# Kernel tuning notes

Measured on AMD Instinct MI355X. Metric: run time of the kernel, lower is better.

## Reference

```python
import jax, jax.numpy as jnp
import numpy as np

B, S, D, K = 16, 4096, 256, 1024


def setup_inputs() -> dict:
    key = jax.random.key(0)
    k1, k2 = jax.random.split(key)
    z_e = jax.random.normal(k1, (B, S, D), dtype=jnp.float32)
    # nn.Embedding weight initialized uniform(-1/K, 1/K)
    codebook = jax.random.uniform(k2, (K, D), dtype=jnp.float32,
                                  minval=-1.0 / K, maxval=1.0 / K)
    return {"z_e": z_e, "codebook": codebook}


def reference(z_e, codebook):
    # straight_through path of VQEmbedding
    d = codebook.shape[1]
    x = z_e.reshape(-1, d)                                   # [N, D]
    dist = (jnp.sum(x * x, axis=1, keepdims=True)
            + jnp.sum(codebook * codebook, axis=1)
            - 2.0 * (x @ codebook.T))                        # [N, K]
    idx = jnp.argmin(dist, axis=1)                           # [N]
    codes = jnp.take(codebook, idx, axis=0).reshape(z_e.shape)  # gather
    z_q = z_e + jax.lax.stop_gradient(codes - z_e)           # straight-through codes (detached codebook)
    z_q_bar = codes                                          # codes with grad to codebook
    return (z_q, z_q_bar)
```

## Files before the change

kernel.cpp:

```cpp
#include <hip/hip_runtime.h>
#include <stdint.h>

#define D 256
#define KCODES 1024
#define NROWS 65536

using int4v  = __attribute__((ext_vector_type(4))) int;
using int16v = __attribute__((ext_vector_type(16))) int;

__device__ __forceinline__ float rne_f(float x) { return __builtin_rintf(x); }

__device__ __forceinline__ void gl_lds16(const void* g, void* l) {
  __builtin_amdgcn_global_load_lds(
      (const __attribute__((address_space(1))) void*)g,
      (__attribute__((address_space(3))) void*)l, 16, 0, 0);
}

__device__ __forceinline__ void dig4(float t, int* d) {
  float f0 = rne_f(t);  float t1 = __fmul_rn(__fsub_rn(t, f0), 256.0f);
  float f1 = rne_f(t1); float t2 = __fmul_rn(__fsub_rn(t1, f1), 256.0f);
  float f2 = rne_f(t2); float t3 = __fmul_rn(__fsub_rn(t2, f2), 256.0f);
  float f3 = rne_f(t3);
  int d0 = (int)f0, d1 = (int)f1, d2 = (int)f2, d3 = (int)f3;
  if (d3 == 128) { d3 = -128; ++d2; }
  if (d2 == 128) { d2 = -128; ++d1; }
  if (d1 == 128) { d1 = -128; ++d0; }
  d[0] = d0; d[1] = d1; d[2] = d2; d[3] = d3;
}

__device__ __forceinline__ float np_block128_sumsq(const float* __restrict__ q) {
  float r[8], v[8];
  *(float4*)(v) = *(const float4*)(q);
  *(float4*)(v + 4) = *(const float4*)(q + 4);
#pragma unroll
  for (int j = 0; j < 8; ++j) r[j] = __fmul_rn(v[j], v[j]);
  for (int i = 8; i < 128; i += 8) {
    *(float4*)(v) = *(const float4*)(q + i);
    *(float4*)(v + 4) = *(const float4*)(q + i + 4);
#pragma unroll
    for (int j = 0; j < 8; ++j) r[j] = __fadd_rn(r[j], __fmul_rn(v[j], v[j]));
  }
  float t01 = __fadd_rn(r[0], r[1]);
  float t23 = __fadd_rn(r[2], r[3]);
  float t45 = __fadd_rn(r[4], r[5]);
  float t67 = __fadd_rn(r[6], r[7]);
  return __fadd_rn(__fadd_rn(t01, t23), __fadd_rn(t45, t67));
}
__device__ __forceinline__ float np_sumsq256(const float* __restrict__ q) {
  return __fadd_rn(np_block128_sumsq(q), np_block128_sumsq(q + 128));
}

__global__ void prep_sums(const float* __restrict__ z, const float* __restrict__ cb,
                          float* __restrict__ c2, float* __restrict__ srow) {
  int r = blockIdx.x * blockDim.x + threadIdx.x;
  if (r < NROWS) srow[r] = np_sumsq256(z + (size_t)r * D);
  else if (r < NROWS + KCODES) c2[r - NROWS] = np_sumsq256(cb + (size_t)(r - NROWS) * D);
}

__global__ void prep_cbdig(const float* __restrict__ cb, char* __restrict__ cbd) {
  int id = blockIdx.x * blockDim.x + threadIdx.x;
  int n = id >> 4, kc = id & 15;
  int f = kc >> 2, kg = kc & 3, nt = n >> 5, c = n & 31;
  const float* src = cb + (size_t)n * D + kc * 16;
  float v[16];
  *(float4*)(v) = *(const float4*)(src);
  *(float4*)(v + 4) = *(const float4*)(src + 4);
  *(float4*)(v + 8) = *(const float4*)(src + 8);
  *(float4*)(v + 12) = *(const float4*)(src + 12);
  int dg[16][4];
#pragma unroll
  for (int e = 0; e < 16; ++e) dig4(v[e] * 65536.0f, dg[e]);
  size_t base = (size_t)nt * 8192 + f * 2048 + (c >> 4) * 1024 + kg * 256 + (c & 15) * 16;
#pragma unroll
  for (int p = 0; p < 4; ++p) {
    int4v wv;
#pragma unroll
    for (int wi = 0; wi < 4; ++wi)
      wv[wi] = (dg[wi * 4][p] & 255) | ((dg[wi * 4 + 1][p] & 255) << 8) |
               ((dg[wi * 4 + 2][p] & 255) << 16) | (dg[wi * 4 + 3][p] << 24);
    *(int4v*)(cbd + (size_t)p * (KCODES * 256) + base) = wv;
  }
}

#define BM 128
#define BN 32
#define NT (KCODES / BN)

#define MFI32(a, b, c) __builtin_amdgcn_mfma_i32_32x32x32_i8((a), (b), (c), 0, 0, 0)

__global__ __launch_bounds__(256, 1) void vq_mfma(
    const float* __restrict__ z, const float* __restrict__ cb,
    const float* __restrict__ c2g, const float* __restrict__ srowg,
    const char* __restrict__ cbd, float* __restrict__ out) {
  __shared__ alignas(16) char bbuf[2][32768];
  __shared__ float c2s[KCODES];
  __shared__ float srow_s[BM];
  __shared__ int bidx_s[BM];

  const int tid = threadIdx.x;
  const int lane = tid & 63;
  const int w = tid >> 6;
  const int r0 = blockIdx.x * BM;
  const int l31 = lane & 31, hi = lane >> 5;

  c2s[tid] = c2g[tid];
  c2s[tid + 256] = c2g[tid + 256];
  c2s[tid + 512] = c2g[tid + 512];
  c2s[tid + 768] = c2g[tid + 768];
  if (tid < BM) srow_s[tid] = srowg[r0 + tid];

  int4v Adig[4][8];
  {
    const float* zr = z + (size_t)(r0 + w * 32 + l31) * D + hi * 16;
#pragma unroll
    for (int kf = 0; kf < 8; ++kf) {
      float v[16];
      *(float4*)(v) = *(const float4*)(zr + kf * 32);
      *(float4*)(v + 4) = *(const float4*)(zr + kf * 32 + 4);
      *(float4*)(v + 8) = *(const float4*)(zr + kf * 32 + 8);
      *(float4*)(v + 12) = *(const float4*)(zr + kf * 32 + 12);
      int dg[16][4];
#pragma unroll
      for (int e = 0; e < 16; ++e) dig4(v[e] * 16.0f, dg[e]);
#pragma unroll
      for (int p = 0; p < 4; ++p) {
        int4v wv;
#pragma unroll
        for (int wi = 0; wi < 4; ++wi)
          wv[wi] = (dg[wi * 4][p] & 255) | ((dg[wi * 4 + 1][p] & 255) << 8) |
                   ((dg[wi * 4 + 2][p] & 255) << 16) | (dg[wi * 4 + 3][p] << 24);
        Adig[p][kf] = wv;
      }
    }
  }

  const char* cbd_b = cbd;
#define STAGE_ALL(ntv, dstbase) do { \
    const char* s_ = cbd_b + (size_t)(ntv) * 8192 + tid * 16; \
    char* d_ = (dstbase) + tid * 16; \
    gl_lds16(s_,          d_);          gl_lds16(s_ + 4096,   d_ + 4096); \
    gl_lds16(s_ + 262144, d_ + 8192);   gl_lds16(s_ + 266240, d_ + 12288); \
    gl_lds16(s_ + 524288, d_ + 16384);  gl_lds16(s_ + 528384, d_ + 20480); \
    gl_lds16(s_ + 786432, d_ + 24576);  gl_lds16(s_ + 790528, d_ + 28672); \
  } while (0)

  const int laneoff = ((lane >> 4) & 1) * 1024 + hi * 256 + (lane & 15) * 16;

  float bd[16]; int bi[16];
#pragma unroll
  for (int r = 0; r < 16; ++r) { bd[r] = 3.4e38f; bi[r] = 0x7fffffff; }

  int16v acc[4];

  STAGE_ALL(0, &bbuf[0][0]);
  __syncthreads();

  for (int nt = 0; nt < NT; ++nt) {
    const char* cur = &bbuf[nt & 1][0];
    if (nt + 1 < NT) STAGE_ALL(nt + 1, &bbuf[(nt + 1) & 1][0]);
#pragma unroll
    for (int s = 0; s < 4; ++s) {
      int16v zz = {0};
      acc[s] = zz;
    }
#pragma unroll
    for (int j = 0; j < 4; ++j) {
#pragma unroll
      for (int kf = 0; kf < 8; ++kf) {
        int4v B = *(const int4v*)(cur + j * 8192 + (kf >> 1) * 2048 + (kf & 1) * 512 + laneoff);
        acc[j + 0] = MFI32(Adig[0][kf], B, acc[j + 0]);
        if (j < 3) acc[j + 1] = MFI32(Adig[1][kf], B, acc[j + 1]);
        if (j < 2) acc[j + 2] = MFI32(Adig[2][kf], B, acc[j + 2]);
        if (j < 1) acc[j + 3] = MFI32(Adig[3][kf], B, acc[j + 3]);
      }
    }
    {
      const int kc = nt * BN + l31;
      const float c2v = c2s[kc];
#pragma unroll
      for (int r = 0; r < 16; ++r) {
        double md = fma(fma(fma((double)acc[0][r], 256.0, (double)acc[1][r]),
                            256.0, (double)acc[2][r]),
                        256.0, (double)acc[3][r]) * 0x1p-44;
        float mf = (float)md;
        const int row_l = w * 32 + (r & 3) + ((r >> 2) << 3) + (hi << 2);
        float dist = __fsub_rn(__fadd_rn(srow_s[row_l], c2v), __fmul_rn(2.0f, mf));
        if (dist < bd[r]) { bd[r] = dist; bi[r] = kc; }
      }
    }
    __syncthreads();
  }

#pragma unroll
  for (int r = 0; r < 16; ++r) {
#pragma unroll
    for (int m = 1; m < 32; m <<= 1) {
      float od = __shfl_xor(bd[r], m);
      int oi = __shfl_xor(bi[r], m);
      if (od < bd[r] || (od == bd[r] && oi < bi[r])) { bd[r] = od; bi[r] = oi; }
    }
    if (l31 == 0) bidx_s[w * 32 + (r & 3) + ((r >> 2) << 3) + (hi << 2)] = bi[r];
  }
  __syncthreads();

  {
    float* out0 = out;
    float* out1 = out + (size_t)NROWS * D;
#pragma unroll
    for (int rr = 0; rr < 32; ++rr) {
      const int row_l = w * 32 + rr;
      const int grow = r0 + row_l;
      const int kb = bidx_s[row_l];
      float4 c4 = *(const float4*)(cb + (size_t)kb * D + lane * 4);
      float4 z4 = *(const float4*)(z + (size_t)grow * D + lane * 4);
      float4 q;
      q.x = __fadd_rn(z4.x, __fsub_rn(c4.x, z4.x));
      q.y = __fadd_rn(z4.y, __fsub_rn(c4.y, z4.y));
      q.z = __fadd_rn(z4.z, __fsub_rn(c4.z, z4.z));
      q.w = __fadd_rn(z4.w, __fsub_rn(c4.w, z4.w));
      *(float4*)(out0 + (size_t)grow * D + lane * 4) = q;
      *(float4*)(out1 + (size_t)grow * D + lane * 4) = c4;
    }
  }
}

__global__ void c2_kernel_fb(const float* __restrict__ cb, float* __restrict__ c2) {
  int k = blockIdx.x * blockDim.x + threadIdx.x;
  if (k < KCODES) c2[k] = np_sumsq256(cb + (size_t)k * D);
}

__global__ __launch_bounds__(256) void vq_fallback(const float* __restrict__ z,
                                                   const float* __restrict__ cb,
                                                   const float* __restrict__ c2,
                                                   float* __restrict__ out) {
  __shared__ float zs[64][260];
  __shared__ float cs[64][260];
  __shared__ float srow[64];
  __shared__ int bidx[64];
  const int tid = threadIdx.x;
  const int tx = tid & 15, ty = tid >> 4;
  const int r0 = blockIdx.x * 64;
#pragma unroll
  for (int it = 0; it < 16; ++it) {
    int g = tid + it * 256, row = g >> 6, f4 = g & 63;
    *(float4*)(&zs[row][f4 * 4]) = *(const float4*)(z + (size_t)(r0 + row) * D + f4 * 4);
  }
  __syncthreads();
  if (tid < 64) srow[tid] = np_sumsq256(&zs[tid][0]);
  float bd[4]; int bi[4];
#pragma unroll
  for (int j = 0; j < 4; ++j) { bd[j] = 3.4e38f; bi[j] = 0x7fffffff; }
  for (int t = 0; t < KCODES / 64; ++t) {
    __syncthreads();
#pragma unroll
    for (int it = 0; it < 16; ++it) {
      int g = tid + it * 256, row = g >> 6, f4 = g & 63;
      *(float4*)(&cs[row][f4 * 4]) = *(const float4*)(cb + (size_t)(t * 64 + row) * D + f4 * 4);
    }
    __syncthreads();
    double acc[4][4];
#pragma unroll
    for (int j = 0; j < 4; ++j)
#pragma unroll
      for (int i = 0; i < 4; ++i) acc[j][i] = 0.0;
#pragma unroll 2
    for (int d = 0; d < D; d += 4) {
      float4 a[4], b[4];
#pragma unroll
      for (int j = 0; j < 4; ++j) a[j] = *(const float4*)(&zs[ty + 16 * j][d]);
#pragma unroll
      for (int i = 0; i < 4; ++i) b[i] = *(const float4*)(&cs[tx + 16 * i][d]);
#pragma unroll
      for (int j = 0; j < 4; ++j)
#pragma unroll
        for (int i = 0; i < 4; ++i) {
          acc[j][i] += (double)a[j].x * (double)b[i].x;
          acc[j][i] += (double)a[j].y * (double)b[i].y;
          acc[j][i] += (double)a[j].z * (double)b[i].z;
          acc[j][i] += (double)a[j].w * (double)b[i].w;
        }
    }
#pragma unroll
    for (int j = 0; j < 4; ++j) {
      const float s = srow[ty + 16 * j];
#pragma unroll
      for (int i = 0; i < 4; ++i) {
        const int k = t * 64 + tx + 16 * i;
        const float m = (float)acc[j][i];
        const float dist = __fsub_rn(__fadd_rn(s, c2[k]), __fmul_rn(2.0f, m));
        if (dist < bd[j]) { bd[j] = dist; bi[j] = k; }
      }
    }
  }
  __syncthreads();
  float* red_d = &cs[0][0];
  int* red_i = (int*)&cs[20][0];
#pragma unroll
  for (int j = 0; j < 4; ++j) {
    red_d[(ty + 16 * j) * 16 + tx] = bd[j];
    red_i[(ty + 16 * j) * 16 + tx] = bi[j];
  }
  __syncthreads();
  if (tid < 64) {
    float best = red_d[tid * 16 + 0];
    int bsti = red_i[tid * 16 + 0];
    for (int x = 1; x < 16; ++x) {
      float d2 = red_d[tid * 16 + x]; int i2 = red_i[tid * 16 + x];
      if (d2 < best || (d2 == best && i2 < bsti)) { best = d2; bsti = i2; }
    }
    bidx[tid] = bsti;
  }
  __syncthreads();
  const int wid = tid >> 6, lane = tid & 63;
  float* out0 = out;
  float* out1 = out + (size_t)NROWS * D;
  for (int r = wid; r < 64; r += 4) {
    const int gr = r0 + r;
    const int kb = bidx[r];
    float4 c4 = *(const float4*)(cb + (size_t)kb * D + lane * 4);
    float4 z4 = *(const float4*)(&zs[r][lane * 4]);
    float4 q;
    q.x = __fadd_rn(z4.x, __fsub_rn(c4.x, z4.x));
    q.y = __fadd_rn(z4.y, __fsub_rn(c4.y, z4.y));
    q.z = __fadd_rn(z4.z, __fsub_rn(c4.z, z4.z));
    q.w = __fadd_rn(z4.w, __fsub_rn(c4.w, z4.w));
    *(float4*)(out0 + (size_t)gr * D + lane * 4) = q;
    *(float4*)(out1 + (size_t)gr * D + lane * 4) = c4;
  }
}

extern "C" void kernel_launch(void* const* d_in, const int* in_sizes, int n_in,
                              void* d_out, int out_size, void* d_ws, size_t ws_size,
                              hipStream_t stream) {
  const float* z = (const float*)d_in[0];
  const float* cb = (const float*)d_in[1];
  float* out = (float*)d_out;

  const size_t c2_off = 0;
  const size_t srow_off = 4096;
  const size_t cbd_off = 4096 + 262144;
  const size_t need = cbd_off + (size_t)4 * KCODES * 256;

  if (ws_size < need) {
    float* c2 = (float*)d_ws;
    c2_kernel_fb<<<KCODES / 256, 256, 0, stream>>>(cb, c2);
    vq_fallback<<<NROWS / 64, 256, 0, stream>>>(z, cb, c2, out);
    return;
  }

  float* c2 = (float*)((char*)d_ws + c2_off);
  float* srow = (float*)((char*)d_ws + srow_off);
  char* cbd = (char*)d_ws + cbd_off;

  prep_sums<<<(NROWS + KCODES) / 256, 256, 0, stream>>>(z, cb, c2, srow);
  prep_cbdig<<<(KCODES * 16) / 256, 256, 0, stream>>>(cb, cbd);
  vq_mfma<<<NROWS / BM, 256, 0, stream>>>(z, cb, c2, srow, cbd, out);
}
```

Measured before the change: 207.9 us.

## Fuse prep kernels, software-pipeline MFMA tiles, int-combine digits, nontemporal output stores

Merges the two prep kernels into one launch. Row sums are now computed from coalesced LDS-staged tiles instead of one thread striding a whole row. The main loop is split into compute/finalize with two accumulator sets, so the argmin epilogue of one tile overlaps the MFMAs of the next. The MFMA issue order is interleaved to reduce dependency stalls, and digit products are combined in int32 before one double FMA. Output stores become nontemporal. The cost is higher register pressure from the doubled accumulators and possible int overflow risk in the digit combine.

```diff
diff --git a/kernel.cpp b/kernel.cpp
--- a/kernel.cpp
+++ b/kernel.cpp
@@ -7,6 +7,7 @@
 
 using int4v  = __attribute__((ext_vector_type(4))) int;
 using int16v = __attribute__((ext_vector_type(16))) int;
+using f32x4v = __attribute__((ext_vector_type(4))) float;
 
 __device__ __forceinline__ float rne_f(float x) { return __builtin_rintf(x); }
 
@@ -50,15 +51,28 @@
   return __fadd_rn(np_block128_sumsq(q), np_block128_sumsq(q + 128));
 }
 
-__global__ void prep_sums(const float* __restrict__ z, const float* __restrict__ cb,
-                          float* __restrict__ c2, float* __restrict__ srow) {
-  int r = blockIdx.x * blockDim.x + threadIdx.x;
-  if (r < NROWS) srow[r] = np_sumsq256(z + (size_t)r * D);
-  else if (r < NROWS + KCODES) c2[r - NROWS] = np_sumsq256(cb + (size_t)(r - NROWS) * D);
-}
-
-__global__ void prep_cbdig(const float* __restrict__ cb, char* __restrict__ cbd) {
-  int id = blockIdx.x * blockDim.x + threadIdx.x;
+__global__ __launch_bounds__(256) void prep_all(const float* __restrict__ z,
+                                                const float* __restrict__ cb,
+                                                float* __restrict__ c2,
+                                                float* __restrict__ srow,
+                                                char* __restrict__ cbd) {
+  __shared__ float zs[64][260];
+  const int bid = blockIdx.x;
+  const int tid = threadIdx.x;
+  if (bid < 1040) {
+    const float* src; float* dst; int r0;
+    if (bid < 1024) { r0 = bid * 64; src = z; dst = srow; }
+    else            { r0 = (bid - 1024) * 64; src = cb; dst = c2; }
+#pragma unroll
+    for (int it = 0; it < 16; ++it) {
+      int g = tid + it * 256, row = g >> 6, f4 = g & 63;
+      *(float4*)(&zs[row][f4 * 4]) = *(const float4*)(src + (size_t)(r0 + row) * D + f4 * 4);
+    }
+    __syncthreads();
+    if (tid < 64) dst[r0 + tid] = np_sumsq256(&zs[tid][0]);
+    return;
+  }
+  int id = (bid - 1040) * 256 + tid;
   int n = id >> 4, kc = id & 15;
   int f = kc >> 2, kg = kc & 3, nt = n >> 5, c = n & 31;
   const float* src = cb + (size_t)n * D + kc * 16;
@@ -88,6 +102,49 @@
 
 #define MFI32(a, b, c) __builtin_amdgcn_mfma_i32_32x32x32_i8((a), (b), (c), 0, 0, 0)
 
+__device__ __forceinline__ void compute_tile(const char* buf, const int4v (&Ad)[4][8],
+                                             int laneoff, int16v (&acc)[4]) {
+#pragma unroll
+  for (int s = 0; s < 4; ++s) { int16v zz = {0}; acc[s] = zz; }
+#pragma unroll
+  for (int kf = 0; kf < 8; ++kf) {
+    const char* pb = buf + (kf >> 1) * 2048 + (kf & 1) * 512 + laneoff;
+    int4v B0 = *(const int4v*)(pb);
+    int4v B1 = *(const int4v*)(pb + 8192);
+    int4v B2 = *(const int4v*)(pb + 16384);
+    int4v B3 = *(const int4v*)(pb + 24576);
+    acc[1] = MFI32(Ad[0][kf], B1, acc[1]);
+    acc[3] = MFI32(Ad[0][kf], B3, acc[3]);
+    acc[2] = MFI32(Ad[0][kf], B2, acc[2]);
+    acc[1] = MFI32(Ad[1][kf], B0, acc[1]);
+    acc[3] = MFI32(Ad[1][kf], B2, acc[3]);
+    acc[2] = MFI32(Ad[1][kf], B1, acc[2]);
+    acc[0] = MFI32(Ad[0][kf], B0, acc[0]);
+    acc[3] = MFI32(Ad[2][kf], B1, acc[3]);
+    acc[2] = MFI32(Ad[2][kf], B0, acc[2]);
+    acc[3] = MFI32(Ad[3][kf], B0, acc[3]);
+  }
+}
+
+__device__ __forceinline__ void finalize_tile(const int16v (&acc)[4], int t,
+                                              int w, int l31, int hi,
+                                              const float* __restrict__ srow_s,
+                                              const float* __restrict__ c2s,
+                                              float (&bd)[16], int (&bi)[16]) {
+  const int kc = t * BN + l31;
+  const float c2v = c2s[kc];
+#pragma unroll
+  for (int r = 0; r < 16; ++r) {
+    int hi32 = acc[0][r] * 256 + acc[1][r];
+    int lo32 = acc[2][r] * 256 + acc[3][r];
+    double md = fma((double)hi32, 65536.0, (double)lo32) * 0x1p-44;
+    float mf = (float)md;
+    const int row_l = w * 32 + (r & 3) + ((r >> 2) << 3) + (hi << 2);
+    float dist = __fsub_rn(__fadd_rn(srow_s[row_l], c2v), __fmul_rn(2.0f, mf));
+    if (dist < bd[r]) { bd[r] = dist; bi[r] = kc; }
+  }
+}
+
 __global__ __launch_bounds__(256, 1) void vq_mfma(
     const float* __restrict__ z, const float* __restrict__ cb,
     const float* __restrict__ c2g, const float* __restrict__ srowg,
@@ -150,46 +207,30 @@
 #pragma unroll
   for (int r = 0; r < 16; ++r) { bd[r] = 3.4e38f; bi[r] = 0x7fffffff; }
 
-  int16v acc[4];
-
-  STAGE_ALL(0, &bbuf[0][0]);
-  __syncthreads();
-
-  for (int nt = 0; nt < NT; ++nt) {
-    const char* cur = &bbuf[nt & 1][0];
-    if (nt + 1 < NT) STAGE_ALL(nt + 1, &bbuf[(nt + 1) & 1][0]);
-#pragma unroll
-    for (int s = 0; s < 4; ++s) {
-      int16v zz = {0};
-      acc[s] = zz;
-    }
-#pragma unroll
-    for (int j = 0; j < 4; ++j) {
-#pragma unroll
-      for (int kf = 0; kf < 8; ++kf) {
-        int4v B = *(const int4v*)(cur + j * 8192 + (kf >> 1) * 2048 + (kf & 1) * 512 + laneoff);
-        acc[j + 0] = MFI32(Adig[0][kf], B, acc[j + 0]);
-        if (j < 3) acc[j + 1] = MFI32(Adig[1][kf], B, acc[j + 1]);
-        if (j < 2) acc[j + 2] = MFI32(Adig[2][kf], B, acc[j + 2]);
-        if (j < 1) acc[j + 3] = MFI32(Adig[3][kf], B, acc[j + 3]);
-      }
-    }
-    {
-      const int kc = nt * BN + l31;
-      const float c2v = c2s[kc];
-#pragma unroll
-      for (int r = 0; r < 16; ++r) {
-        double md = fma(fma(fma((double)acc[0][r], 256.0, (double)acc[1][r]),
-                            256.0, (double)acc[2][r]),
-                        256.0, (double)acc[3][r]) * 0x1p-44;
-        float mf = (float)md;
-        const int row_l = w * 32 + (r & 3) + ((r >> 2) << 3) + (hi << 2);
-        float dist = __fsub_rn(__fadd_rn(srow_s[row_l], c2v), __fmul_rn(2.0f, mf));
-        if (dist < bd[r]) { bd[r] = dist; bi[r] = kc; }
-      }
-    }
-    __syncthreads();
-  }
+  int16v accA[4], accB[4];
+  char* b0 = &bbuf[0][0];
+  char* b1 = &bbuf[1][0];
+
+  STAGE_ALL(0, b0);
+  __syncthreads();
+
+  STAGE_ALL(1, b1);
+  compute_tile(b0, Adig, laneoff, accA);
+  __syncthreads();
+
+  for (int t = 1; t + 1 < NT; t += 2) {
+    STAGE_ALL(t + 1, b0);
+    compute_tile(b1, Adig, laneoff, accB);
+    finalize_tile(accA, t - 1, w, l31, hi, srow_s, c2s, bd, bi);
+    __syncthreads();
+    STAGE_ALL(t + 2, b1);
+    compute_tile(b0, Adig, laneoff, accA);
+    finalize_tile(accB, t, w, l31, hi, srow_s, c2s, bd, bi);
+    __syncthreads();
+  }
+  compute_tile(b1, Adig, laneoff, accB);
+  finalize_tile(accA, NT - 2, w, l31, hi, srow_s, c2s, bd, bi);
+  finalize_tile(accB, NT - 1, w, l31, hi, srow_s, c2s, bd, bi);
 
 #pragma unroll
   for (int r = 0; r < 16; ++r) {
@@ -211,15 +252,15 @@
       const int row_l = w * 32 + rr;
       const int grow = r0 + row_l;
       const int kb = bidx_s[row_l];
-      float4 c4 = *(const float4*)(cb + (size_t)kb * D + lane * 4);
-      float4 z4 = *(const float4*)(z + (size_t)grow * D + lane * 4);
-      float4 q;
+      f32x4v c4 = *(const f32x4v*)(cb + (size_t)kb * D + lane * 4);
+      f32x4v z4 = *(const f32x4v*)(z + (size_t)grow * D + lane * 4);
+      f32x4v q;
       q.x = __fadd_rn(z4.x, __fsub_rn(c4.x, z4.x));
       q.y = __fadd_rn(z4.y, __fsub_rn(c4.y, z4.y));
       q.z = __fadd_rn(z4.z, __fsub_rn(c4.z, z4.z));
       q.w = __fadd_rn(z4.w, __fsub_rn(c4.w, z4.w));
-      *(float4*)(out0 + (size_t)grow * D + lane * 4) = q;
-      *(float4*)(out1 + (size_t)grow * D + lane * 4) = c4;
+      __builtin_nontemporal_store(q, (f32x4v*)(out0 + (size_t)grow * D + lane * 4));
+      __builtin_nontemporal_store(c4, (f32x4v*)(out1 + (size_t)grow * D + lane * 4));
     }
   }
 }
@@ -352,7 +393,6 @@
   float* srow = (float*)((char*)d_ws + srow_off);
   char* cbd = (char*)d_ws + cbd_off;
 
-  prep_sums<<<(NROWS + KCODES) / 256, 256, 0, stream>>>(z, cb, c2, srow);
-  prep_cbdig<<<(KCODES * 16) / 256, 256, 0, stream>>>(cb, cbd);
+  prep_all<<<1104, 256, 0, stream>>>(z, cb, c2, srow, cbd);
   vq_mfma<<<NROWS / BM, 256, 0, stream>>>(z, cb, c2, srow, cbd, out);
 }
```

After: 223.1 us. 7.3% more time.
